# Kernel optimization log

Measured on AMD Instinct MI355X. Metric: run time of the kernel, lower is better.

The kernel has to match this reference:

```python
import jax, jax.numpy as jnp
import numpy as np

B, NNEG, D, E = 16384, 10, 8, 64
N_ENT = 500000  # sum(domain_dims.values())
N_PAIRS = D * (D - 1) // 2


def setup_inputs() -> dict:
    key = jax.random.key(0)
    k1, k2, k3, k4, k5 = jax.random.split(key, 5)
    return {
        "pos_x": jax.random.randint(k1, (B, D), 0, N_ENT, dtype=jnp.int32),
        "neg_x": jax.random.randint(k2, (B, NNEG, D), 0, N_ENT, dtype=jnp.int32),
        "emb_table": jax.random.normal(k3, (N_ENT, E), dtype=jnp.float32) * 0.01,
        "pair_w": jax.random.uniform(k4, (N_PAIRS,), dtype=jnp.float32),
        "c": jax.random.uniform(k5, (1,), dtype=jnp.float32),
    }


def _obtain_score(x, emb_table, pair_w, c):
    # x: [..., D] int indices into the shared embedding table
    e = emb_table[x]                                   # [..., D, E] gather
    gram = jnp.einsum('...de,...fe->...df', e, e)      # [..., D, D] pairwise dots
    iu, ju = np.triu_indices(D, k=1)
    pair_dots = gram[..., iu, ju]                      # [..., N_PAIRS]
    # NOTE: the original torch code never increments k inside obtain_score,
    # so EVERY pair is scaled by exp(pair_W['0']). We replicate that faithfully.
    r = pair_dots * jnp.exp(pair_w[0])
    return jnp.exp(jnp.sum(r, axis=-1) + c[0])         # [...]


def reference(pos_x, neg_x, emb_table, pair_w, c):
    pos_score = _obtain_score(pos_x, emb_table, pair_w, c)   # [B]
    # vectorized over the negative-sample axis (original loops in Python)
    neg_score = _obtain_score(neg_x, emb_table, pair_w, c)   # [B, NNEG]
    return pos_score, neg_score
```

## Files before the change

kernel.cpp:

```cpp
#include <hip/hip_runtime.h>

constexpr int B     = 16384;
constexpr int NNEG  = 10;
constexpr int D     = 8;
constexpr int E     = 64;
constexpr int ROWS  = B * (1 + NNEG);
constexpr int RPW   = 4;

__global__ __launch_bounds__(256) void APE_61555471286335_kernel(
    const int*   __restrict__ pos_x,
    const int*   __restrict__ neg_x,
    const float* __restrict__ emb,
    const float* __restrict__ pair_w,
    const float* __restrict__ c,
    float*       __restrict__ out)
{
    const int tid  = blockIdx.x * blockDim.x + threadIdx.x;
    const int wave = tid >> 6;
    const int lane = threadIdx.x & 63;
    const int row0 = wave * RPW;

    float v[RPW][D];
#pragma unroll
    for (int r = 0; r < RPW; ++r) {
        const int row = row0 + r;
        const int* idx = (row < B) ? (pos_x + (size_t)row * D)
                                   : (neg_x + (size_t)(row - B) * D);
#pragma unroll
        for (int d = 0; d < D; ++d) {
            v[r][d] = emb[(size_t)idx[d] * E + lane];
        }
    }

    float p[RPW];
#pragma unroll
    for (int r = 0; r < RPW; ++r) {
        float s = 0.f, ss = 0.f;
#pragma unroll
        for (int d = 0; d < D; ++d) {
            s  += v[r][d];
            ss += v[r][d] * v[r][d];
        }
        p[r] = s * s - ss;
    }

#pragma unroll
    for (int off = 32; off > 0; off >>= 1) {
#pragma unroll
        for (int r = 0; r < RPW; ++r)
            p[r] += __shfl_xor(p[r], off, 64);
    }

    if (lane == 0) {
        const float w = expf(pair_w[0]);
        const float cc = c[0];
#pragma unroll
        for (int r = 0; r < RPW; ++r)
            out[row0 + r] = expf(0.5f * p[r] * w + cc);
    }
}

extern "C" void kernel_launch(void* const* d_in, const int* in_sizes, int n_in,
                              void* d_out, int out_size, void* d_ws, size_t ws_size,
                              hipStream_t stream) {
    const int*   pos_x  = (const int*)  d_in[0];
    const int*   neg_x  = (const int*)  d_in[1];
    const float* emb    = (const float*)d_in[2];
    const float* pair_w = (const float*)d_in[3];
    const float* c      = (const float*)d_in[4];
    float*       out    = (float*)      d_out;

    constexpr int BLOCK = 256;
    constexpr int ROWS_PER_BLOCK = (BLOCK / 64) * RPW;
    static_assert(ROWS % ROWS_PER_BLOCK == 0, "exact grid");
    const int grid = ROWS / ROWS_PER_BLOCK;

    APE_61555471286335_kernel<<<grid, BLOCK, 0, stream>>>(
        pos_x, neg_x, emb, pair_w, c, out);
}
```

Baseline: 212.5 us.

## Map 16 lanes per row with float4 gathers and vectorized index loads

Each wave now handles 8 rows, with 16 lanes per row each loading a float4 slice of the embedding, in place of 64 lanes each loading one scalar. Index rows are read as two int4 loads, so there are fewer memory instructions and the reduction shrinks to 4 shuffle steps. The grid halves because rows per block double, which lowers the number of waves available to hide gather latency.

Result: no change. 213.3 us (+0.3%).

```diff
diff --git a/kernel.cpp b/kernel.cpp
--- a/kernel.cpp
+++ b/kernel.cpp
@@ -5,7 +5,7 @@
 constexpr int D     = 8;
 constexpr int E     = 64;
 constexpr int ROWS  = B * (1 + NNEG);
-constexpr int RPW   = 4;
+constexpr int RPW   = 8;
 
 __global__ __launch_bounds__(256) void APE_61555471286335_kernel(
     const int*   __restrict__ pos_x,
@@ -18,45 +18,56 @@
     const int tid  = blockIdx.x * blockDim.x + threadIdx.x;
     const int wave = tid >> 6;
     const int lane = threadIdx.x & 63;
+    const int g    = lane >> 4;
+    const int t    = lane & 15;
     const int row0 = wave * RPW;
+    const int rowA = row0 + g;
+    const int rowB = row0 + 4 + g;
 
-    float v[RPW][D];
+    const int* idxA = (rowA < B) ? (pos_x + (size_t)rowA * D)
+                                 : (neg_x + (size_t)(rowA - B) * D);
+    const int* idxB = (rowB < B) ? (pos_x + (size_t)rowB * D)
+                                 : (neg_x + (size_t)(rowB - B) * D);
+    const int4 a0 = *(const int4*)(idxA), a1 = *(const int4*)(idxA + 4);
+    const int4 b0 = *(const int4*)(idxB), b1 = *(const int4*)(idxB + 4);
+    const int idA[D] = {a0.x, a0.y, a0.z, a0.w, a1.x, a1.y, a1.z, a1.w};
+    const int idB[D] = {b0.x, b0.y, b0.z, b0.w, b1.x, b1.y, b1.z, b1.w};
+
+    float4 vA[D], vB[D];
 #pragma unroll
-    for (int r = 0; r < RPW; ++r) {
-        const int row = row0 + r;
-        const int* idx = (row < B) ? (pos_x + (size_t)row * D)
-                                   : (neg_x + (size_t)(row - B) * D);
+    for (int d = 0; d < D; ++d)
+        vA[d] = *(const float4*)(emb + (size_t)idA[d] * E + t * 4);
 #pragma unroll
-        for (int d = 0; d < D; ++d) {
-            v[r][d] = emb[(size_t)idx[d] * E + lane];
-        }
+    for (int d = 0; d < D; ++d)
+        vB[d] = *(const float4*)(emb + (size_t)idB[d] * E + t * 4);
+
+    float4 sA = make_float4(0.f, 0.f, 0.f, 0.f), qA = sA;
+    float4 sB = sA, qB = sA;
+#pragma unroll
+    for (int d = 0; d < D; ++d) {
+        sA.x += vA[d].x; sA.y += vA[d].y; sA.z += vA[d].z; sA.w += vA[d].w;
+        qA.x += vA[d].x * vA[d].x; qA.y += vA[d].y * vA[d].y;
+        qA.z += vA[d].z * vA[d].z; qA.w += vA[d].w * vA[d].w;
+        sB.x += vB[d].x; sB.y += vB[d].y; sB.z += vB[d].z; sB.w += vB[d].w;
+        qB.x += vB[d].x * vB[d].x; qB.y += vB[d].y * vB[d].y;
+        qB.z += vB[d].z * vB[d].z; qB.w += vB[d].w * vB[d].w;
+    }
+    float pA = sA.x * sA.x + sA.y * sA.y + sA.z * sA.z + sA.w * sA.w
+             - (qA.x + qA.y + qA.z + qA.w);
+    float pB = sB.x * sB.x + sB.y * sB.y + sB.z * sB.z + sB.w * sB.w
+             - (qB.x + qB.y + qB.z + qB.w);
+
+#pragma unroll
+    for (int off = 8; off > 0; off >>= 1) {
+        pA += __shfl_xor(pA, off, 64);
+        pB += __shfl_xor(pB, off, 64);
     }
 
-    float p[RPW];
-#pragma unroll
-    for (int r = 0; r < RPW; ++r) {
-        float s = 0.f, ss = 0.f;
-#pragma unroll
-        for (int d = 0; d < D; ++d) {
-            s  += v[r][d];
-            ss += v[r][d] * v[r][d];
-        }
-        p[r] = s * s - ss;
-    }
-
-#pragma unroll
-    for (int off = 32; off > 0; off >>= 1) {
-#pragma unroll
-        for (int r = 0; r < RPW; ++r)
-            p[r] += __shfl_xor(p[r], off, 64);
-    }
-
-    if (lane == 0) {
-        const float w = expf(pair_w[0]);
+    if (t == 0) {
+        const float w  = expf(pair_w[0]);
         const float cc = c[0];
-#pragma unroll
-        for (int r = 0; r < RPW; ++r)
-            out[row0 + r] = expf(0.5f * p[r] * w + cc);
+        out[rowA] = expf(0.5f * pA * w + cc);
+        out[rowB] = expf(0.5f * pB * w + cc);
     }
 }
 
```
